# Kernel tuning notes

Measured on AMD Instinct MI355X. Metric: run time of the kernel, lower is better.

The kernel has to match this reference:

```python
import jax, jax.numpy as jnp
import numpy as np
from jax import lax

C_IN, C_OUT, K = 32, 32, 3
DIV = float(np.sqrt(C_IN * K * K))  # sqrt(channels_in * filter_size^2)


def setup_inputs() -> dict:
    key = jax.random.key(0)
    kx, kw = jax.random.split(key)
    x = jax.random.normal(kx, (32, C_IN, 256, 256), dtype=jnp.float32)  # NCHW
    # torch.normal(0.0, 0.01, (Cout, Cin, k, k))
    weight = 0.01 * jax.random.normal(kw, (C_OUT, C_IN, K, K), dtype=jnp.float32)
    return {"x": x, "weight": weight}


def reference(x, weight):
    # binarize weights: sign with 0 -> -1 (torch.where(x > 0, 1.0, -1.0))
    weight_bin = jnp.where(weight > 0, 1.0, -1.0).astype(weight.dtype)
    # conv2d with 'same' padding (padding = k // 2, stride 1)
    out = lax.conv_general_dilated(
        x, weight_bin,
        window_strides=(1, 1),
        padding=((K // 2, K // 2), (K // 2, K // 2)),
        dimension_numbers=("NCHW", "OIHW", "NCHW"),
    )
    return out / DIV
```

## Files before the change

kernel.cpp:

```cpp
#include <hip/hip_runtime.h>


typedef __attribute__((ext_vector_type(8))) short short8;
typedef __attribute__((ext_vector_type(4))) float f32x4;

__device__ __forceinline__ short bf16s(float f) {
    unsigned int u = __builtin_bit_cast(unsigned int, f);
    u += 0x7FFFu + ((u >> 16) & 1u);
    return (short)(u >> 16);
}

__global__ __launch_bounds__(512, 4)
void bconv2d_kernel(const float* __restrict__ x, const float* __restrict__ wgt,
                    float* __restrict__ out) {
    __shared__ short8 lds[4 * 1032];

    const int tid = threadIdx.x;
    const int y0  = blockIdx.x * 16;
    const int n   = blockIdx.y;

    const int l      = tid & 63;
    const int wv     = tid >> 6;
    const int seg    = wv >> 1;
    const int ch     = wv & 1;
    const int px0    = seg * 64;
    const int lane15 = l & 15;
    const int lhi    = l >> 4;

    short8 afrag[3][3];
    {
        const int co  = ch * 16 + lane15;
        const int ci0 = lhi * 8;
        #pragma unroll
        for (int dy = 0; dy < 3; ++dy)
            #pragma unroll
            for (int dx = 0; dx < 3; ++dx) {
                short8 a;
                #pragma unroll
                for (int j = 0; j < 8; ++j) {
                    float wval = wgt[((co * 32 + ci0 + j) * 3 + dy) * 3 + dx];
                    a[j] = (short)((wval > 0.0f) ? 0x3F80 : 0xBF80);
                }
                afrag[dy][dx] = a;
            }
    }

    const float* xn = x + (size_t)n * 32 * 65536;

    float rg[2][8];

    auto load_row = [&](int gy) {
        if ((unsigned)gy < 256u) {
            #pragma unroll
            for (int k = 0; k < 2; ++k) {
                const int t  = tid + k * 512;
                const int u  = t >> 8;
                const int gx = t & 255;
                const float* src = xn + ((size_t)(u * 8) * 256 + gy) * 256 + gx;
                #pragma unroll
                for (int j = 0; j < 8; ++j) rg[k][j] = src[(size_t)j * 65536];
            }
        } else {
            #pragma unroll
            for (int k = 0; k < 2; ++k)
                #pragma unroll
                for (int j = 0; j < 8; ++j) rg[k][j] = 0.0f;
        }
    };

    auto write_row = [&](int slot) {
        #pragma unroll
        for (int k = 0; k < 2; ++k) {
            const int t  = tid + k * 512;
            const int u  = t >> 8;
            const int pl = 1 + (t & 255);
            short8 v;
            #pragma unroll
            for (int j = 0; j < 8; ++j) v[j] = bf16s(rg[k][j]);
            lds[slot * 1032 + pl * 4 + (u ^ ((pl >> 1) & 3))] = v;
        }
    };

    load_row(y0 - 1); write_row((y0 - 1) & 3);
    load_row(y0);     write_row(y0 & 3);
    load_row(y0 + 1); write_row((y0 + 1) & 3);
    if (tid < 32) {
        const int slot = tid & 3;
        const int u    = (tid >> 2) & 3;
        const int pl   = (tid >> 4) ? 257 : 0;
        lds[slot * 1032 + pl * 4 + u] = (short8)0;
    }
    __syncthreads();

    const float invdiv = 0.05892556509887896f;

    #pragma unroll 4
    for (int yy = 0; yy < 16; ++yy) {
        const int y = y0 + yy;

        load_row(y + 2);

        f32x4 acc[4];
        #pragma unroll
        for (int tp = 0; tp < 4; ++tp) acc[tp] = (f32x4)0.0f;

        #pragma unroll
        for (int ss = 0; ss < 3; ++ss) {
            const int m     = (yy + ss + 3) & 3;
            const int sbase = m * 1032;
            #pragma unroll
            for (int dx = 0; dx < 3; ++dx)
                #pragma unroll
                for (int tp = 0; tp < 4; ++tp) {
                    const int pl = px0 + tp * 16 + lane15 + dx;
                    short8 b = lds[sbase + pl * 4 + (lhi ^ ((pl >> 1) & 3))];
                    acc[tp] = __builtin_amdgcn_mfma_f32_16x16x32_bf16(
                        afrag[ss][dx], b, acc[tp], 0, 0, 0);
                }
        }

        write_row((yy + 2) & 3);

        #pragma unroll
        for (int tp = 0; tp < 4; ++tp)
            #pragma unroll
            for (int q = 0; q < 4; ++q) {
                const int co = ch * 16 + lhi * 4 + q;
                out[(((size_t)n * 32 + co) * 256 + y) * 256 + px0 + tp * 16 + lane15]
                    = acc[tp][q] * invdiv;
            }

        __syncthreads();
    }
}

extern "C" void kernel_launch(void* const* d_in, const int* in_sizes, int n_in,
                              void* d_out, int out_size, void* d_ws, size_t ws_size,
                              hipStream_t stream) {
    const float* x   = (const float*)d_in[0];
    const float* wgt = (const float*)d_in[1];
    float* out = (float*)d_out;
    (void)d_ws; (void)ws_size;
    dim3 grid(16, 32);
    dim3 block(512);
    bconv2d_kernel<<<grid, block, 0, stream>>>(x, wgt, out);
}
```

Baseline: 140.0 us.

## Split width into 128-pixel tiles and double-buffer row loads over six LDS slots

The kernel now tiles each image row into two 128-pixel halves handled by separate blocks, with a few threads loading the left and right halo columns. This doubles the grid and shrinks per-block LDS so more blocks fit per CU. The row ring grows from 4 to 6 slots, and two register buffers let global loads for rows y+4/y+5 run while the MFMA compute for the current rows proceeds. In exchange, the halo columns are read twice, the launch bound rises to 6 waves per SIMD, and the new edge-thread logic adds branching.

```diff
diff --git a/kernel.cpp b/kernel.cpp
--- a/kernel.cpp
+++ b/kernel.cpp
@@ -10,20 +10,21 @@
     return (short)(u >> 16);
 }
 
-__global__ __launch_bounds__(512, 4)
+__global__ __launch_bounds__(512, 6)
 void bconv2d_kernel(const float* __restrict__ x, const float* __restrict__ wgt,
                     float* __restrict__ out) {
-    __shared__ short8 lds[4 * 1032];
+    __shared__ short8 lds[6 * 528];
 
     const int tid = threadIdx.x;
-    const int y0  = blockIdx.x * 16;
-    const int n   = blockIdx.y;
+    const int x0  = blockIdx.x * 128;
+    const int y0  = blockIdx.y * 16;
+    const int n   = blockIdx.z;
 
     const int l      = tid & 63;
     const int wv     = tid >> 6;
     const int seg    = wv >> 1;
     const int ch     = wv & 1;
-    const int px0    = seg * 64;
+    const int px0    = seg * 32;
     const int lane15 = l & 15;
     const int lhi    = l >> 4;
 
@@ -47,90 +48,120 @@
 
     const float* xn = x + (size_t)n * 32 * 65536;
 
-    float rg[2][8];
+    const int iu  = tid >> 7;
+    const int igx = x0 + (tid & 127);
+    const bool is_edge = (tid >= 480) && (tid < 488);
+    const int  eside   = tid & 1;
+    const int  eu      = (tid - 480) >> 1;
+    const int  egx     = eside ? x0 + 128 : x0 - 1;
 
-    auto load_row = [&](int gy) {
+    float rgA[8], rgB[8], reA[8], reB[8];
+
+    auto load_row = [&](int gy, float (&rg)[8], float (&re)[8]) {
         if ((unsigned)gy < 256u) {
+            const float* src = xn + ((size_t)(iu * 8) * 256 + gy) * 256 + igx;
             #pragma unroll
-            for (int k = 0; k < 2; ++k) {
-                const int t  = tid + k * 512;
-                const int u  = t >> 8;
-                const int gx = t & 255;
-                const float* src = xn + ((size_t)(u * 8) * 256 + gy) * 256 + gx;
-                #pragma unroll
-                for (int j = 0; j < 8; ++j) rg[k][j] = src[(size_t)j * 65536];
-            }
+            for (int j = 0; j < 8; ++j) rg[j] = src[(size_t)j * 65536];
         } else {
             #pragma unroll
-            for (int k = 0; k < 2; ++k)
+            for (int j = 0; j < 8; ++j) rg[j] = 0.0f;
+        }
+        if (is_edge) {
+            if ((unsigned)gy < 256u && (unsigned)egx < 256u) {
+                const float* src = xn + ((size_t)(eu * 8) * 256 + gy) * 256 + egx;
                 #pragma unroll
-                for (int j = 0; j < 8; ++j) rg[k][j] = 0.0f;
+                for (int j = 0; j < 8; ++j) re[j] = src[(size_t)j * 65536];
+            } else {
+                #pragma unroll
+                for (int j = 0; j < 8; ++j) re[j] = 0.0f;
+            }
         }
     };
 
-    auto write_row = [&](int slot) {
+    auto write_row = [&](int slot, float (&rg)[8], float (&re)[8]) {
+        const int pl = 1 + (tid & 127);
+        short8 v;
         #pragma unroll
-        for (int k = 0; k < 2; ++k) {
-            const int t  = tid + k * 512;
-            const int u  = t >> 8;
-            const int pl = 1 + (t & 255);
-            short8 v;
+        for (int j = 0; j < 8; ++j) v[j] = bf16s(rg[j]);
+        lds[slot * 528 + pl * 4 + (iu ^ ((pl >> 1) & 3))] = v;
+        if (is_edge) {
+            const int ple = eside ? 129 : 0;
+            short8 w;
             #pragma unroll
-            for (int j = 0; j < 8; ++j) v[j] = bf16s(rg[k][j]);
-            lds[slot * 1032 + pl * 4 + (u ^ ((pl >> 1) & 3))] = v;
+            for (int j = 0; j < 8; ++j) w[j] = bf16s(re[j]);
+            lds[slot * 528 + ple * 4 + (eu ^ ((ple >> 1) & 3))] = w;
         }
     };
 
-    load_row(y0 - 1); write_row((y0 - 1) & 3);
-    load_row(y0);     write_row(y0 & 3);
-    load_row(y0 + 1); write_row((y0 + 1) & 3);
-    if (tid < 32) {
-        const int slot = tid & 3;
-        const int u    = (tid >> 2) & 3;
-        const int pl   = (tid >> 4) ? 257 : 0;
-        lds[slot * 1032 + pl * 4 + u] = (short8)0;
-    }
-    __syncthreads();
-
     const float invdiv = 0.05892556509887896f;
 
-    #pragma unroll 4
-    for (int yy = 0; yy < 16; ++yy) {
-        const int y = y0 + yy;
-
-        load_row(y + 2);
-
-        f32x4 acc[4];
+    auto row_cs = [&](int yy, int s0, int s1, int s2) {
+        f32x4 acc[2];
+        acc[0] = (f32x4)0.0f;
+        acc[1] = (f32x4)0.0f;
+        const int sb[3] = {s0 * 528, s1 * 528, s2 * 528};
         #pragma unroll
-        for (int tp = 0; tp < 4; ++tp) acc[tp] = (f32x4)0.0f;
-
-        #pragma unroll
-        for (int ss = 0; ss < 3; ++ss) {
-            const int m     = (yy + ss + 3) & 3;
-            const int sbase = m * 1032;
+        for (int ss = 0; ss < 3; ++ss)
             #pragma unroll
             for (int dx = 0; dx < 3; ++dx)
                 #pragma unroll
-                for (int tp = 0; tp < 4; ++tp) {
+                for (int tp = 0; tp < 2; ++tp) {
                     const int pl = px0 + tp * 16 + lane15 + dx;
-                    short8 b = lds[sbase + pl * 4 + (lhi ^ ((pl >> 1) & 3))];
+                    short8 b = lds[sb[ss] + pl * 4 + (lhi ^ ((pl >> 1) & 3))];
                     acc[tp] = __builtin_amdgcn_mfma_f32_16x16x32_bf16(
                         afrag[ss][dx], b, acc[tp], 0, 0, 0);
                 }
-        }
-
-        write_row((yy + 2) & 3);
-
+        const int y = y0 + yy;
         #pragma unroll
-        for (int tp = 0; tp < 4; ++tp)
+        for (int tp = 0; tp < 2; ++tp)
             #pragma unroll
             for (int q = 0; q < 4; ++q) {
                 const int co = ch * 16 + lhi * 4 + q;
-                out[(((size_t)n * 32 + co) * 256 + y) * 256 + px0 + tp * 16 + lane15]
+                out[(((size_t)n * 32 + co) * 256 + y) * 256 + x0 + px0 + tp * 16 + lane15]
                     = acc[tp][q] * invdiv;
             }
+    };
 
+    load_row(y0 - 1, rgA, reA); write_row(0, rgA, reA);
+    load_row(y0,     rgA, reA); write_row(1, rgA, reA);
+    load_row(y0 + 1, rgA, reA); write_row(2, rgA, reA);
+    load_row(y0 + 2, rgA, reA);
+    load_row(y0 + 3, rgB, reB);
+    __syncthreads();
+
+    int s = 0;
+    #pragma unroll 1
+    for (int it = 0; it < 6; ++it) {
+        const int yy = 2 * it;
+        const int t0 = s, t1 = (s + 1 < 6) ? s + 1 : s - 5,
+                  t2 = (s + 2 < 6) ? s + 2 : s - 4,
+                  t3 = (s + 3 < 6) ? s + 3 : s - 3,
+                  t4 = (s + 4 < 6) ? s + 4 : s - 2;
+        write_row(t3, rgA, reA);
         __syncthreads();
+        load_row(y0 + yy + 4, rgA, reA);
+        row_cs(yy, t0, t1, t2);
+        write_row(t4, rgB, reB);
+        __syncthreads();
+        load_row(y0 + yy + 5, rgB, reB);
+        row_cs(yy + 1, t1, t2, t3);
+        s = (s + 2 < 6) ? s + 2 : s - 4;
+    }
+
+    {
+        const int t0 = 0, t1 = 1, t2 = 2, t3 = 3, t4 = 4, t5 = 5;
+        write_row(t3, rgA, reA);
+        __syncthreads();
+        load_row(y0 + 16, rgA, reA);
+        row_cs(12, t0, t1, t2);
+        write_row(t4, rgB, reB);
+        __syncthreads();
+        row_cs(13, t1, t2, t3);
+        write_row(t5, rgA, reA);
+        __syncthreads();
+        row_cs(14, t2, t3, t4);
+        __syncthreads();
+        row_cs(15, t3, t4, t5);
     }
 }
 
@@ -141,7 +172,7 @@
     const float* wgt = (const float*)d_in[1];
     float* out = (float*)d_out;
     (void)d_ws; (void)ws_size;
-    dim3 grid(16, 32);
+    dim3 grid(2, 16, 32);
     dim3 block(512);
     bconv2d_kernel<<<grid, block, 0, stream>>>(x, wgt, out);
 }
```

Result: slower. 434.0 us (+210.0%).

## Switch to 32x32x16 MFMA with each wave covering all 32 output channels

Applied to the files above, without the earlier changes.

Replaces the four 16x16x32 bf16 MFMAs per tap with two 32x32x16 MFMAs. Each wave now owns 32 pixels across all 32 output channels instead of 64 pixels across 16 channels, which halves the LDS B-fragment reads per MFMA and changes how weights are split across waves. It also swaps __syncthreads for an explicit lgkmcnt wait plus s_barrier and sets the row loop to unroll 1. Lighter synchronisation risks ordering bugs, and the new output stores are 32 lanes wide per channel.

```diff
diff --git a/kernel.cpp b/kernel.cpp
--- a/kernel.cpp
+++ b/kernel.cpp
@@ -2,7 +2,7 @@
 
 
 typedef __attribute__((ext_vector_type(8))) short short8;
-typedef __attribute__((ext_vector_type(4))) float f32x4;
+typedef __attribute__((ext_vector_type(16))) float f32x16;
 
 __device__ __forceinline__ short bf16s(float f) {
     unsigned int u = __builtin_bit_cast(unsigned int, f);
@@ -19,30 +19,29 @@
     const int y0  = blockIdx.x * 16;
     const int n   = blockIdx.y;
 
-    const int l      = tid & 63;
-    const int wv     = tid >> 6;
-    const int seg    = wv >> 1;
-    const int ch     = wv & 1;
-    const int px0    = seg * 64;
-    const int lane15 = l & 15;
-    const int lhi    = l >> 4;
+    const int l   = tid & 63;
+    const int wv  = tid >> 6;
+    const int px0 = wv * 32;
+    const int l31 = l & 31;
+    const int lh  = l >> 5;
 
-    short8 afrag[3][3];
+    short8 afrag[3][3][2];
     {
-        const int co  = ch * 16 + lane15;
-        const int ci0 = lhi * 8;
         #pragma unroll
         for (int dy = 0; dy < 3; ++dy)
             #pragma unroll
-            for (int dx = 0; dx < 3; ++dx) {
-                short8 a;
+            for (int dx = 0; dx < 3; ++dx)
                 #pragma unroll
-                for (int j = 0; j < 8; ++j) {
-                    float wval = wgt[((co * 32 + ci0 + j) * 3 + dy) * 3 + dx];
-                    a[j] = (short)((wval > 0.0f) ? 0x3F80 : 0xBF80);
+                for (int kk = 0; kk < 2; ++kk) {
+                    short8 a;
+                    #pragma unroll
+                    for (int j = 0; j < 8; ++j) {
+                        const int ci = kk * 16 + lh * 8 + j;
+                        float wval = wgt[((l31 * 32 + ci) * 3 + dy) * 3 + dx];
+                        a[j] = (short)((wval > 0.0f) ? 0x3F80 : 0xBF80);
+                    }
+                    afrag[dy][dx][kk] = a;
                 }
-                afrag[dy][dx] = a;
-            }
     }
 
     const float* xn = x + (size_t)n * 32 * 65536;
@@ -81,56 +80,54 @@
         }
     };
 
-    load_row(y0 - 1); write_row((y0 - 1) & 3);
-    load_row(y0);     write_row(y0 & 3);
-    load_row(y0 + 1); write_row((y0 + 1) & 3);
+    load_row(y0 - 1); write_row(3);
+    load_row(y0);     write_row(0);
+    load_row(y0 + 1); write_row(1);
     if (tid < 32) {
         const int slot = tid & 3;
         const int u    = (tid >> 2) & 3;
         const int pl   = (tid >> 4) ? 257 : 0;
         lds[slot * 1032 + pl * 4 + u] = (short8)0;
     }
-    __syncthreads();
+    asm volatile("s_waitcnt lgkmcnt(0)" ::: "memory");
+    __builtin_amdgcn_s_barrier();
 
     const float invdiv = 0.05892556509887896f;
 
-    #pragma unroll 4
+    #pragma unroll 1
     for (int yy = 0; yy < 16; ++yy) {
         const int y = y0 + yy;
 
         load_row(y + 2);
 
-        f32x4 acc[4];
-        #pragma unroll
-        for (int tp = 0; tp < 4; ++tp) acc[tp] = (f32x4)0.0f;
-
+        f32x16 acc = (f32x16)0.0f;
         #pragma unroll
         for (int ss = 0; ss < 3; ++ss) {
-            const int m     = (yy + ss + 3) & 3;
-            const int sbase = m * 1032;
+            const int sbase = ((yy + ss + 3) & 3) * 1032;
             #pragma unroll
-            for (int dx = 0; dx < 3; ++dx)
+            for (int dx = 0; dx < 3; ++dx) {
+                const int pl = px0 + l31 + dx;
                 #pragma unroll
-                for (int tp = 0; tp < 4; ++tp) {
-                    const int pl = px0 + tp * 16 + lane15 + dx;
-                    short8 b = lds[sbase + pl * 4 + (lhi ^ ((pl >> 1) & 3))];
-                    acc[tp] = __builtin_amdgcn_mfma_f32_16x16x32_bf16(
-                        afrag[ss][dx], b, acc[tp], 0, 0, 0);
+                for (int kk = 0; kk < 2; ++kk) {
+                    const int u = kk * 2 + lh;
+                    short8 b = lds[sbase + pl * 4 + (u ^ ((pl >> 1) & 3))];
+                    acc = __builtin_amdgcn_mfma_f32_32x32x16_bf16(
+                        afrag[ss][dx][kk], b, acc, 0, 0, 0);
                 }
+            }
         }
 
         write_row((yy + 2) & 3);
 
         #pragma unroll
-        for (int tp = 0; tp < 4; ++tp)
-            #pragma unroll
-            for (int q = 0; q < 4; ++q) {
-                const int co = ch * 16 + lhi * 4 + q;
-                out[(((size_t)n * 32 + co) * 256 + y) * 256 + px0 + tp * 16 + lane15]
-                    = acc[tp][q] * invdiv;
-            }
+        for (int q = 0; q < 16; ++q) {
+            const int co = (q & 3) + 8 * (q >> 2) + 4 * lh;
+            out[(((size_t)n * 32 + co) * 256 + y) * 256 + px0 + l31]
+                = acc[q] * invdiv;
+        }
 
-        __syncthreads();
+        asm volatile("s_waitcnt lgkmcnt(0)" ::: "memory");
+        __builtin_amdgcn_s_barrier();
     }
 }
 
```

New measurement: 163.2 us. +16.6%, slower.

## Double-buffer input row prefetch two rows ahead with lightweight LDS barriers

Applied to the files above, without the earlier changes.

Input rows are now prefetched into two alternating register buffers, so global loads run two rows ahead of the MFMA compute instead of one. The LDS write for the next row moves before the compute, which the 4-slot ring buffer allows. The loop is manually unrolled by two. __syncthreads is replaced with an lgkmcnt(0) wait plus s_barrier, so the barrier does not wait on outstanding global loads. The extra 16 floats of prefetch state raise register pressure under launch_bounds(512,4) and could cause spills or lower occupancy.

```diff
diff --git a/kernel.cpp b/kernel.cpp
--- a/kernel.cpp
+++ b/kernel.cpp
@@ -8,6 +8,11 @@
     unsigned int u = __builtin_bit_cast(unsigned int, f);
     u += 0x7FFFu + ((u >> 16) & 1u);
     return (short)(u >> 16);
+}
+
+__device__ __forceinline__ void lgkm_barrier() {
+    asm volatile("s_waitcnt lgkmcnt(0)" ::: "memory");
+    __builtin_amdgcn_s_barrier();
 }
 
 __global__ __launch_bounds__(512, 4)
@@ -47,9 +52,9 @@
 
     const float* xn = x + (size_t)n * 32 * 65536;
 
-    float rg[2][8];
+    float rgA[2][8], rgB[2][8];
 
-    auto load_row = [&](int gy) {
+    auto load_row = [&](int gy, float (&rg)[2][8]) {
         if ((unsigned)gy < 256u) {
             #pragma unroll
             for (int k = 0; k < 2; ++k) {
@@ -68,7 +73,7 @@
         }
     };
 
-    auto write_row = [&](int slot) {
+    auto write_row = [&](int slot, float (&rg)[2][8]) {
         #pragma unroll
         for (int k = 0; k < 2; ++k) {
             const int t  = tid + k * 512;
@@ -81,33 +86,16 @@
         }
     };
 
-    load_row(y0 - 1); write_row((y0 - 1) & 3);
-    load_row(y0);     write_row(y0 & 3);
-    load_row(y0 + 1); write_row((y0 + 1) & 3);
-    if (tid < 32) {
-        const int slot = tid & 3;
-        const int u    = (tid >> 2) & 3;
-        const int pl   = (tid >> 4) ? 257 : 0;
-        lds[slot * 1032 + pl * 4 + u] = (short8)0;
-    }
-    __syncthreads();
-
     const float invdiv = 0.05892556509887896f;
 
-    #pragma unroll 4
-    for (int yy = 0; yy < 16; ++yy) {
+    auto row_cs = [&](int yy) {
         const int y = y0 + yy;
-
-        load_row(y + 2);
-
         f32x4 acc[4];
         #pragma unroll
         for (int tp = 0; tp < 4; ++tp) acc[tp] = (f32x4)0.0f;
-
         #pragma unroll
         for (int ss = 0; ss < 3; ++ss) {
-            const int m     = (yy + ss + 3) & 3;
-            const int sbase = m * 1032;
+            const int sbase = ((yy + ss + 3) & 3) * 1032;
             #pragma unroll
             for (int dx = 0; dx < 3; ++dx)
                 #pragma unroll
@@ -118,9 +106,6 @@
                         afrag[ss][dx], b, acc[tp], 0, 0, 0);
                 }
         }
-
-        write_row((yy + 2) & 3);
-
         #pragma unroll
         for (int tp = 0; tp < 4; ++tp)
             #pragma unroll
@@ -129,8 +114,34 @@
                 out[(((size_t)n * 32 + co) * 256 + y) * 256 + px0 + tp * 16 + lane15]
                     = acc[tp][q] * invdiv;
             }
+    };
 
-        __syncthreads();
+    load_row(y0 - 1, rgA); write_row(3, rgA);
+    load_row(y0,     rgA); write_row(0, rgA);
+    load_row(y0 + 1, rgA); write_row(1, rgA);
+    load_row(y0 + 2, rgA);
+    load_row(y0 + 3, rgB);
+    if (tid < 32) {
+        const int slot = tid & 3;
+        const int u    = (tid >> 2) & 3;
+        const int pl   = (tid >> 4) ? 257 : 0;
+        lds[slot * 1032 + pl * 4 + u] = (short8)0;
+    }
+    lgkm_barrier();
+
+    #pragma unroll 1
+    for (int ii = 0; ii < 8; ++ii) {
+        const int ye = 2 * ii;
+        write_row((ye + 2) & 3, rgA);
+        if (ii <= 6) load_row(y0 + ye + 4, rgA);
+        row_cs(ye);
+        lgkm_barrier();
+
+        const int yo = ye + 1;
+        if (ii <= 6) write_row((yo + 2) & 3, rgB);
+        if (ii <= 5) load_row(y0 + yo + 4, rgB);
+        row_cs(yo);
+        lgkm_barrier();
     }
 }
 
```

Result: slower. 148.8 us (+6.3%).
